# Kernel optimization log

Hardware: AMD Instinct MI355X
Metric: run time of the kernel (lower is better)

Reference implementation:

```python
import jax, jax.numpy as jnp
import numpy as np

H = W = 240

def setup_inputs() -> dict:
    key = jax.random.key(0)
    k1, k2, k3 = jax.random.split(key, 3)
    B = 256
    T2_Gen = jax.random.normal(k1, (B, 1, H, W), dtype=jnp.float32)
    underT2_K = jax.random.normal(k2, (B, 2, H, W), dtype=jnp.float32)
    # k-space sampling mask (soft in [0,1); original uses a fixed undersampling mask)
    A = jax.random.uniform(k3, (H, W), dtype=jnp.float32)
    return {"T2_Gen": T2_Gen, "underT2_K": underT2_K, "A": A}

def reference(T2_Gen, underT2_K, A):
    # x2: [B, H, W]
    x2 = T2_Gen.reshape(-1, H, W)
    # batched 2D FFT over the last two axes (replaces the per-slice numpy loop)
    x2_k = jnp.fft.fft2(x2)  # complex64
    # undersampled k-space as complex: real = channel 0, imag = channel 1
    y_k = underT2_K[:, 0, :, :] + 1j * underT2_K[:, 1, :, :]
    z_k = (1.0 - A) * x2_k + y_k
    z = jnp.abs(jnp.fft.ifft2(z_k))  # [B, H, W] real
    return z.reshape(-1, 1, H, W)
```

## Files before the change

### kernel.cpp

```cpp
#include <hip/hip_runtime.h>
#include <hip/hip_fp16.h>
#include <math.h>

#define HW 240
#define PITCH 241
#define IMG_PIX (HW*HW)
#define NB 15
#define TILE_ELEMS (240*16)

__device__ __forceinline__ float2 cmul(float2 a, float2 b){
    return make_float2(a.x*b.x - a.y*b.y, a.x*b.y + a.y*b.x);
}
__device__ __forceinline__ float2 cadd(float2 a, float2 b){
    return make_float2(a.x+b.x, a.y+b.y);
}
__device__ __forceinline__ float2 csub(float2 a, float2 b){
    return make_float2(a.x-b.x, a.y-b.y);
}
__device__ __forceinline__ __half2 f2h(float2 a){ return __floats2half2_rn(a.x, a.y); }
__device__ __forceinline__ float2 h2f(__half2 h){ return make_float2(__low2float(h), __high2float(h)); }

template<int SIGN>
__device__ __forceinline__ void dft15(const float2* x, float2* X){
    const float S = (float)SIGN;
    const float s3 = 0.8660254037844387f;
    float2 y[5][3];
    #pragma unroll
    for (int n2 = 0; n2 < 5; ++n2){
        float2 a0 = x[n2], a1 = x[5+n2], a2 = x[10+n2];
        float2 t = cadd(a1, a2);
        float2 u = csub(a1, a2);
        float2 m = make_float2(a0.x - 0.5f*t.x, a0.y - 0.5f*t.y);
        float sx = S * s3;
        float2 s = make_float2(-sx*u.y, sx*u.x);
        y[n2][0] = cadd(a0, t);
        y[n2][1] = cadd(m, s);
        y[n2][2] = csub(m, s);
    }
    const float C15[9] = {1.f, 0.9135454576426009f, 0.6691306063588582f, 0.30901699437494745f,
                          -0.10452846326765346f, -0.5f, -0.8090169943749475f,
                          -0.9781476007338057f, -0.9781476007338057f};
    const float S15[9] = {0.f, 0.4067366430758004f, 0.7431448254773942f, 0.9510565162951535f,
                          0.9945218953682733f, 0.8660254037844387f, 0.5877852522924731f,
                          0.20791169081775931f, -0.20791169081775931f};
    #pragma unroll
    for (int n2 = 1; n2 < 5; ++n2){
        #pragma unroll
        for (int k1 = 1; k1 < 3; ++k1){
            const int e = n2*k1;
            y[n2][k1] = cmul(y[n2][k1], make_float2(C15[e], S*S15[e]));
        }
    }
    const float c1 = 0.30901699437494745f, s1 = 0.9510565162951535f;
    const float c2 = -0.8090169943749475f, s2 = 0.5877852522924731f;
    #pragma unroll
    for (int k1 = 0; k1 < 3; ++k1){
        float2 x0 = y[0][k1], x1 = y[1][k1], x2 = y[2][k1], x3 = y[3][k1], x4 = y[4][k1];
        float2 t1 = cadd(x1, x4), t3 = csub(x1, x4);
        float2 t2 = cadd(x2, x3), t4 = csub(x2, x3);
        X[k1] = make_float2(x0.x + t1.x + t2.x, x0.y + t1.y + t2.y);
        float2 u1 = make_float2(x0.x + c1*t1.x + c2*t2.x, x0.y + c1*t1.y + c2*t2.y);
        float2 u2 = make_float2(x0.x + c2*t1.x + c1*t2.x, x0.y + c2*t1.y + c1*t2.y);
        float2 v1 = make_float2(S*(s1*t3.x + s2*t4.x), S*(s1*t3.y + s2*t4.y));
        float2 v2 = make_float2(S*(s2*t3.x - s1*t4.x), S*(s2*t3.y - s1*t4.y));
        X[k1+3]  = make_float2(u1.x - v1.y, u1.y + v1.x);
        X[k1+12] = make_float2(u1.x + v1.y, u1.y - v1.x);
        X[k1+6]  = make_float2(u2.x - v2.y, u2.y + v2.x);
        X[k1+9]  = make_float2(u2.x + v2.y, u2.y - v2.x);
    }
}

template<int SIGN>
__device__ __forceinline__ void dft16(const float2* x, float2* X){
    const float S = (float)SIGN;
    float2 y[4][4];
    #pragma unroll
    for (int n2 = 0; n2 < 4; ++n2){
        float2 a0 = x[n2], a1 = x[4+n2], a2 = x[8+n2], a3 = x[12+n2];
        float2 t0 = cadd(a0,a2), t1 = csub(a0,a2);
        float2 t2 = cadd(a1,a3), t3 = csub(a1,a3);
        float2 it3 = make_float2(-S*t3.y, S*t3.x);
        y[n2][0] = cadd(t0,t2);
        y[n2][2] = csub(t0,t2);
        y[n2][1] = cadd(t1,it3);
        y[n2][3] = csub(t1,it3);
    }
    const float C16[10] = {1.f, 0.9238795325112867f, 0.7071067811865476f, 0.3826834323650898f,
                           0.f, -0.3826834323650898f, -0.7071067811865476f, -0.9238795325112867f,
                           -1.f, -0.9238795325112867f};
    const float S16[10] = {0.f, 0.3826834323650898f, 0.7071067811865476f, 0.9238795325112867f,
                           1.f, 0.9238795325112867f, 0.7071067811865476f, 0.3826834323650898f,
                           0.f, -0.3826834323650898f};
    #pragma unroll
    for (int n2 = 1; n2 < 4; ++n2){
        #pragma unroll
        for (int k1 = 1; k1 < 4; ++k1){
            const int e = n2*k1;
            y[n2][k1] = cmul(y[n2][k1], make_float2(C16[e], S*S16[e]));
        }
    }
    #pragma unroll
    for (int k1 = 0; k1 < 4; ++k1){
        float2 a0 = y[0][k1], a1 = y[1][k1], a2 = y[2][k1], a3 = y[3][k1];
        float2 t0 = cadd(a0,a2), t1 = csub(a0,a2);
        float2 t2 = cadd(a1,a3), t3 = csub(a1,a3);
        float2 it3 = make_float2(-S*t3.y, S*t3.x);
        X[k1]    = cadd(t0,t2);
        X[k1+8]  = csub(t0,t2);
        X[k1+4]  = cadd(t1,it3);
        X[k1+12] = csub(t1,it3);
    }
}

template<int SIGN>
__device__ __forceinline__ void fft240_wave(float2 (*sm)[PITCH], float2* v, int row, int b){
    const float TWOPI = 6.28318530717958647692f;
    float2 Y[15];
    dft15<SIGN>(v, Y);
    float2 step, tw = make_float2(1.0f, 0.0f);
    {
        float ang = (float)SIGN * TWOPI * (float)b * (1.0f/240.0f);
        __sincosf(ang, &step.y, &step.x);
    }
    #pragma unroll
    for (int d = 0; d < 15; ++d){
        sm[row][b*15 + d] = cmul(Y[d], tw);
        tw = cmul(tw, step);
    }
    __builtin_amdgcn_wave_barrier();
    if (b < 15){
        float2 Z[16];
        #pragma unroll
        for (int bb = 0; bb < 16; ++bb) Z[bb] = sm[row][bb*15 + b];
        float2 XX[16];
        dft16<SIGN>(Z, XX);
        #pragma unroll
        for (int m = 0; m < 16; ++m) sm[row][15*m + b] = XX[m];
    }
    __builtin_amdgcn_wave_barrier();
}

__global__ __launch_bounds__(256) void passA_rowfft(const float* __restrict__ x,
                                                    __half2* __restrict__ out){
    __shared__ float2 sm[16][PITCH];
    float* smf = (float*)sm;
    int g = blockIdx.x, img = g / NB, h0 = (g % NB) * 16;
    int tid = threadIdx.x, wave = tid >> 6, lane = tid & 63;
    int rl4 = lane >> 4, b = lane & 15, row = wave*4 + rl4;
    const float* src = x + (size_t)img * IMG_PIX + (size_t)(h0 + wave*4) * HW;
    #pragma unroll
    for (int i = 0; i < 15; ++i){
        int f = i*64 + lane;
        smf[(wave*4 + f/HW)*(2*PITCH) + (f%HW)] = src[f];
    }
    __builtin_amdgcn_wave_barrier();
    float2 v[15];
    #pragma unroll
    for (int a = 0; a < 15; ++a) v[a] = make_float2(smf[row*(2*PITCH) + 16*a + b], 0.0f);
    __builtin_amdgcn_wave_barrier();
    fft240_wave<-1>(sm, v, row, b);
    #pragma unroll
    for (int kb = 0; kb < NB; ++kb){
        float2 val = sm[row][kb*16 + b];
        out[((size_t)(img*NB + kb)*HW + h0 + wave*4 + rl4)*16 + b] = f2h(val);
    }
}

__global__ __launch_bounds__(256) void passB_col_dc_icol(const __half2* __restrict__ in,
                                                         const float* __restrict__ under,
                                                         const float* __restrict__ Am,
                                                         __half2* __restrict__ out){
    __shared__ float2 sm[16][PITCH];
    int g = blockIdx.x, img = g / NB, s = g % NB, kw0 = s * 16;
    int tid = threadIdx.x, wave = tid >> 6, lane = tid & 63;
    int rl4 = lane >> 4, b = lane & 15, row = wave*4 + rl4;
    const __half2* src = in + (size_t)(img*NB + s) * TILE_ELEMS;
    #pragma unroll
    for (int i = 0; i < 15; ++i){
        int f = i*256 + tid;
        sm[f & 15][f >> 4] = h2f(src[f]);
    }
    __syncthreads();
    float2 v[15];
    #pragma unroll
    for (int a = 0; a < 15; ++a) v[a] = sm[row][16*a + b];
    __builtin_amdgcn_wave_barrier();
    fft240_wave<-1>(sm, v, row, b);
    __syncthreads();

    int rl = tid >> 4, bb = tid & 15;
    const float* y0 = under + (size_t)img * (2*IMG_PIX);
    const float* y1 = y0 + IMG_PIX;
    #pragma unroll
    for (int j = 0; j < 15; ++j){
        int kh = j*16 + rl;
        size_t p = (size_t)kh * HW + kw0 + bb;
        float sc = 1.0f - Am[p];
        float2 X = sm[bb][kh];
        sm[bb][kh] = make_float2(sc * X.x + y0[p], sc * X.y + y1[p]);
    }
    __syncthreads();
    #pragma unroll
    for (int a = 0; a < 15; ++a) v[a] = sm[row][16*a + b];
    __builtin_amdgcn_wave_barrier();
    fft240_wave<+1>(sm, v, row, b);
    __syncthreads();

    const float inv240 = 1.0f / 240.0f;
    __half2* dst = out + (size_t)(img*NB + s) * TILE_ELEMS;
    #pragma unroll
    for (int i = 0; i < 15; ++i){
        int f = i*256 + tid;
        float2 val = sm[f & 15][f >> 4];
        val.x *= inv240; val.y *= inv240;
        dst[f] = f2h(val);
    }
}

__global__ __launch_bounds__(256) void passC_irow_abs(const __half2* __restrict__ in,
                                                      float* __restrict__ outp){
    __shared__ float2 sm[16][PITCH];
    int g = blockIdx.x, img = g / NB, h0 = (g % NB) * 16;
    int tid = threadIdx.x, wave = tid >> 6, lane = tid & 63;
    int rl4 = lane >> 4, b = lane & 15, row = wave*4 + rl4;
    #pragma unroll
    for (int kb = 0; kb < NB; ++kb){
        __half2 hv = in[((size_t)(img*NB + kb)*HW + h0 + wave*4 + rl4)*16 + b];
        sm[row][kb*16 + b] = h2f(hv);
    }
    __builtin_amdgcn_wave_barrier();
    float2 v[15];
    #pragma unroll
    for (int a = 0; a < 15; ++a) v[a] = sm[row][16*a + b];
    __builtin_amdgcn_wave_barrier();
    fft240_wave<+1>(sm, v, row, b);
    float* dst = outp + (size_t)img * IMG_PIX + (size_t)(h0 + wave*4) * HW;
    const float inv240 = 1.0f / 240.0f;
    #pragma unroll
    for (int i = 0; i < 15; ++i){
        int f = i*64 + lane;
        float2 X = sm[wave*4 + f/HW][f%HW];
        dst[f] = sqrtf(X.x*X.x + X.y*X.y) * inv240;
    }
}

extern "C" void kernel_launch(void* const* d_in, const int* in_sizes, int n_in,
                              void* d_out, int out_size, void* d_ws, size_t ws_size,
                              hipStream_t stream){
    const float* T2   = (const float*)d_in[0];
    const float* U    = (const float*)d_in[1];
    const float* Am   = (const float*)d_in[2];
    float* out        = (float*)d_out;

    const int B = 256;
    __half2* i1 = (__half2*)d_ws;
    __half2* i2 = i1 + (size_t)B * IMG_PIX;

    dim3 grid(B * NB), block(256);
    passA_rowfft     <<<grid, block, 0, stream>>>(T2, i1);
    passB_col_dc_icol<<<grid, block, 0, stream>>>(i1, U, Am, i2);
    passC_irow_abs   <<<grid, block, 0, stream>>>(i2, out);
}
```

Before: 284.8 us.

## Store FFT shared-memory staging in half2 and load rows directly from global

Shared-memory tiles in all three passes switch from float2 to __half2, halving LDS footprint and traffic, and launch bounds now request 8 blocks per CU to raise occupancy. Passes A and C drop the shared-memory staging of their input rows and read the needed elements straight from global memory into registers. This trims LDS round trips and barriers but adds more fp16 rounding inside each FFT stage, and the direct global reads are less coalesced.

```diff
diff --git a/kernel.cpp b/kernel.cpp
--- a/kernel.cpp
+++ b/kernel.cpp
@@ -113,7 +113,7 @@
 }
 
 template<int SIGN>
-__device__ __forceinline__ void fft240_wave(float2 (*sm)[PITCH], float2* v, int row, int b){
+__device__ __forceinline__ void fft240_wave(__half2 (*sm)[PITCH], float2* v, int row, int b){
     const float TWOPI = 6.28318530717958647692f;
     float2 Y[15];
     dft15<SIGN>(v, Y);
@@ -124,53 +124,44 @@
     }
     #pragma unroll
     for (int d = 0; d < 15; ++d){
-        sm[row][b*15 + d] = cmul(Y[d], tw);
+        sm[row][b*15 + d] = f2h(cmul(Y[d], tw));
         tw = cmul(tw, step);
     }
     __builtin_amdgcn_wave_barrier();
     if (b < 15){
         float2 Z[16];
         #pragma unroll
-        for (int bb = 0; bb < 16; ++bb) Z[bb] = sm[row][bb*15 + b];
+        for (int bb = 0; bb < 16; ++bb) Z[bb] = h2f(sm[row][bb*15 + b]);
         float2 XX[16];
         dft16<SIGN>(Z, XX);
         #pragma unroll
-        for (int m = 0; m < 16; ++m) sm[row][15*m + b] = XX[m];
-    }
-    __builtin_amdgcn_wave_barrier();
-}
-
-__global__ __launch_bounds__(256) void passA_rowfft(const float* __restrict__ x,
-                                                    __half2* __restrict__ out){
-    __shared__ float2 sm[16][PITCH];
-    float* smf = (float*)sm;
+        for (int m = 0; m < 16; ++m) sm[row][15*m + b] = f2h(XX[m]);
+    }
+    __builtin_amdgcn_wave_barrier();
+}
+
+__global__ __launch_bounds__(256, 8) void passA_rowfft(const float* __restrict__ x,
+                                                       __half2* __restrict__ out){
+    __shared__ __half2 sm[16][PITCH];
     int g = blockIdx.x, img = g / NB, h0 = (g % NB) * 16;
     int tid = threadIdx.x, wave = tid >> 6, lane = tid & 63;
     int rl4 = lane >> 4, b = lane & 15, row = wave*4 + rl4;
-    const float* src = x + (size_t)img * IMG_PIX + (size_t)(h0 + wave*4) * HW;
-    #pragma unroll
-    for (int i = 0; i < 15; ++i){
-        int f = i*64 + lane;
-        smf[(wave*4 + f/HW)*(2*PITCH) + (f%HW)] = src[f];
-    }
-    __builtin_amdgcn_wave_barrier();
+    const float* src = x + (size_t)img * IMG_PIX + (size_t)(h0 + row) * HW;
     float2 v[15];
     #pragma unroll
-    for (int a = 0; a < 15; ++a) v[a] = make_float2(smf[row*(2*PITCH) + 16*a + b], 0.0f);
-    __builtin_amdgcn_wave_barrier();
+    for (int a = 0; a < 15; ++a) v[a] = make_float2(src[16*a + b], 0.0f);
     fft240_wave<-1>(sm, v, row, b);
     #pragma unroll
     for (int kb = 0; kb < NB; ++kb){
-        float2 val = sm[row][kb*16 + b];
-        out[((size_t)(img*NB + kb)*HW + h0 + wave*4 + rl4)*16 + b] = f2h(val);
-    }
-}
-
-__global__ __launch_bounds__(256) void passB_col_dc_icol(const __half2* __restrict__ in,
-                                                         const float* __restrict__ under,
-                                                         const float* __restrict__ Am,
-                                                         __half2* __restrict__ out){
-    __shared__ float2 sm[16][PITCH];
+        out[((size_t)(img*NB + kb)*HW + h0 + row)*16 + b] = sm[row][kb*16 + b];
+    }
+}
+
+__global__ __launch_bounds__(256, 8) void passB_col_dc_icol(const __half2* __restrict__ in,
+                                                            const float* __restrict__ under,
+                                                            const float* __restrict__ Am,
+                                                            __half2* __restrict__ out){
+    __shared__ __half2 sm[16][PITCH];
     int g = blockIdx.x, img = g / NB, s = g % NB, kw0 = s * 16;
     int tid = threadIdx.x, wave = tid >> 6, lane = tid & 63;
     int rl4 = lane >> 4, b = lane & 15, row = wave*4 + rl4;
@@ -178,12 +169,12 @@
     #pragma unroll
     for (int i = 0; i < 15; ++i){
         int f = i*256 + tid;
-        sm[f & 15][f >> 4] = h2f(src[f]);
+        sm[f & 15][f >> 4] = src[f];
     }
     __syncthreads();
     float2 v[15];
     #pragma unroll
-    for (int a = 0; a < 15; ++a) v[a] = sm[row][16*a + b];
+    for (int a = 0; a < 15; ++a) v[a] = h2f(sm[row][16*a + b]);
     __builtin_amdgcn_wave_barrier();
     fft240_wave<-1>(sm, v, row, b);
     __syncthreads();
@@ -196,12 +187,12 @@
         int kh = j*16 + rl;
         size_t p = (size_t)kh * HW + kw0 + bb;
         float sc = 1.0f - Am[p];
-        float2 X = sm[bb][kh];
-        sm[bb][kh] = make_float2(sc * X.x + y0[p], sc * X.y + y1[p]);
-    }
-    __syncthreads();
-    #pragma unroll
-    for (int a = 0; a < 15; ++a) v[a] = sm[row][16*a + b];
+        float2 X = h2f(sm[bb][kh]);
+        sm[bb][kh] = f2h(make_float2(sc * X.x + y0[p], sc * X.y + y1[p]));
+    }
+    __syncthreads();
+    #pragma unroll
+    for (int a = 0; a < 15; ++a) v[a] = h2f(sm[row][16*a + b]);
     __builtin_amdgcn_wave_barrier();
     fft240_wave<+1>(sm, v, row, b);
     __syncthreads();
@@ -211,35 +202,30 @@
     #pragma unroll
     for (int i = 0; i < 15; ++i){
         int f = i*256 + tid;
-        float2 val = sm[f & 15][f >> 4];
+        float2 val = h2f(sm[f & 15][f >> 4]);
         val.x *= inv240; val.y *= inv240;
         dst[f] = f2h(val);
     }
 }
 
-__global__ __launch_bounds__(256) void passC_irow_abs(const __half2* __restrict__ in,
-                                                      float* __restrict__ outp){
-    __shared__ float2 sm[16][PITCH];
+__global__ __launch_bounds__(256, 8) void passC_irow_abs(const __half2* __restrict__ in,
+                                                         float* __restrict__ outp){
+    __shared__ __half2 sm[16][PITCH];
     int g = blockIdx.x, img = g / NB, h0 = (g % NB) * 16;
     int tid = threadIdx.x, wave = tid >> 6, lane = tid & 63;
     int rl4 = lane >> 4, b = lane & 15, row = wave*4 + rl4;
-    #pragma unroll
-    for (int kb = 0; kb < NB; ++kb){
-        __half2 hv = in[((size_t)(img*NB + kb)*HW + h0 + wave*4 + rl4)*16 + b];
-        sm[row][kb*16 + b] = h2f(hv);
-    }
-    __builtin_amdgcn_wave_barrier();
     float2 v[15];
     #pragma unroll
-    for (int a = 0; a < 15; ++a) v[a] = sm[row][16*a + b];
-    __builtin_amdgcn_wave_barrier();
+    for (int a = 0; a < 15; ++a){
+        v[a] = h2f(in[((size_t)(img*NB + a)*HW + h0 + row)*16 + b]);
+    }
     fft240_wave<+1>(sm, v, row, b);
     float* dst = outp + (size_t)img * IMG_PIX + (size_t)(h0 + wave*4) * HW;
     const float inv240 = 1.0f / 240.0f;
     #pragma unroll
     for (int i = 0; i < 15; ++i){
         int f = i*64 + lane;
-        float2 X = sm[wave*4 + f/HW][f%HW];
+        float2 X = h2f(sm[wave*4 + f/HW][f%HW]);
         dst[f] = sqrtf(X.x*X.x + X.y*X.y) * inv240;
     }
 }
```

Measured after the change: 487.6 us. 1.71x slower.
